# Performance work log

Measured on AMD Instinct MI355X. Metric: run time of the kernel, lower is better.

The kernel has to match this reference:

```python
import jax, jax.numpy as jnp
import numpy as np

B, N, IN_F, OUT_F = 32, 1024, 256, 256
ALPHA = 0.2  # LeakyReLU negative slope
NEG_INF = -9e15  # matches torch's -9000000000000000.0 masking constant


def setup_inputs() -> dict:
    key = jax.random.key(0)
    k1, k2, k3, k4 = jax.random.split(key, 4)
    h = jax.random.normal(k1, (B, N, IN_F), dtype=jnp.float32)
    adj = jax.random.randint(k2, (B, N, N), 0, 2, dtype=jnp.int32)
    W = jax.random.normal(k3, (OUT_F, IN_F), dtype=jnp.float32) * 0.05
    a = jax.random.normal(k4, (1, 2 * OUT_F), dtype=jnp.float32) * 0.05
    return {"h": h, "adj": adj, "W": W, "a": a}


def reference(h, adj, W, a):
    # Wh: (B, N, out)
    Wh = jnp.einsum("bni,oi->bno", h, W)
    # Decompose a([Wh_i || Wh_j]) = Wh_i . a1 + Wh_j . a2 (identical math,
    # avoids the O(B*N^2*2*out) concat intermediate of the torch code).
    a1 = a[0, :OUT_F]   # (out,)
    a2 = a[0, OUT_F:]   # (out,)
    si = Wh @ a1        # (B, N) score contribution of source node i
    sj = Wh @ a2        # (B, N) score contribution of neighbor node j
    e = jax.nn.leaky_relu(si[:, :, None] + sj[:, None, :], negative_slope=ALPHA)
    attention = jnp.where(adj > 0, e, NEG_INF)
    attention = jax.nn.softmax(attention, axis=-1)
    # dropout omitted (eval mode)
    h_prime = jnp.einsum("bij,bjo->bio", attention, Wh)
    return jax.nn.elu(h_prime)
```

## Files before the change

kernel.cpp:

```cpp
#include <hip/hip_runtime.h>
#include <hip/hip_bf16.h>


#define ALPHA 0.2f

typedef __bf16 bf16x8 __attribute__((ext_vector_type(8)));
typedef __bf16 bf16x4 __attribute__((ext_vector_type(4)));
typedef float  f32x4  __attribute__((ext_vector_type(4)));
typedef unsigned long long u64;

__global__ __launch_bounds__(256) void k0_mask(const int* __restrict__ adj,
                                               u64* __restrict__ mask) {
    const int wid = (blockIdx.x * 256 + threadIdx.x) >> 6;
    const int l   = threadIdx.x & 63;
    const size_t base = (size_t)wid * 64;
    #pragma unroll 4
    for (int it = 0; it < 64; ++it) {
        const size_t word = base + it;
        const int v = adj[word * 64 + l];
        const u64 m = __ballot(v > 0);
        if (l == 0) mask[word] = m;
    }
}

__global__ __launch_bounds__(256) void k1_gemm1(const float* __restrict__ h,
                                                const float* __restrict__ W,
                                                const float* __restrict__ a_g,
                                                __bf16* __restrict__ whT,
                                                float* __restrict__ si,
                                                float* __restrict__ sj) {
    __shared__ __bf16 hA[64 * 72];
    __shared__ __bf16 hB[256 * 72];
    __shared__ float  red[512];
    const int t    = threadIdx.x;
    const int r0   = blockIdx.x * 64;
    const int b    = r0 >> 10;
    const int n0   = r0 & 1023;
    const int w    = t >> 6;
    const int l    = t & 63;
    const int ln   = l & 15;
    const int quad = l >> 4;

    f32x4 acc[4][4] = {};
    float4 ha_r[4], wb_r[16];

    #pragma unroll
    for (int it = 0; it < 4; ++it)
        ha_r[it] = *(const float4*)&h[(size_t)(r0 + it * 16 + (t >> 4)) * 256 + (t & 15) * 4];
    #pragma unroll
    for (int it = 0; it < 16; ++it)
        wb_r[it] = *(const float4*)&W[(size_t)(it * 16 + (t >> 4)) * 256 + (t & 15) * 4];

    for (int kc = 0; kc < 4; ++kc) {
        #pragma unroll
        for (int it = 0; it < 4; ++it) {
            const float4 v = ha_r[it];
            bf16x4 pv = {(__bf16)v.x, (__bf16)v.y, (__bf16)v.z, (__bf16)v.w};
            *(bf16x4*)&hA[(it * 16 + (t >> 4)) * 72 + (t & 15) * 4] = pv;
        }
        #pragma unroll
        for (int it = 0; it < 16; ++it) {
            const float4 v = wb_r[it];
            bf16x4 pv = {(__bf16)v.x, (__bf16)v.y, (__bf16)v.z, (__bf16)v.w};
            *(bf16x4*)&hB[(it * 16 + (t >> 4)) * 72 + (t & 15) * 4] = pv;
        }
        __syncthreads();
        if (kc < 3) {
            const int k0 = (kc + 1) * 64;
            #pragma unroll
            for (int it = 0; it < 4; ++it)
                ha_r[it] = *(const float4*)&h[(size_t)(r0 + it * 16 + (t >> 4)) * 256 + k0 + (t & 15) * 4];
            #pragma unroll
            for (int it = 0; it < 16; ++it)
                wb_r[it] = *(const float4*)&W[(size_t)(it * 16 + (t >> 4)) * 256 + k0 + (t & 15) * 4];
        }
        #pragma unroll
        for (int kk = 0; kk < 2; ++kk) {
            bf16x8 af[4], bfr[4];
            #pragma unroll
            for (int ri = 0; ri < 4; ++ri)
                af[ri] = *(const bf16x8*)&hA[(ri * 16 + ln) * 72 + kk * 32 + quad * 8];
            #pragma unroll
            for (int oi = 0; oi < 4; ++oi)
                bfr[oi] = *(const bf16x8*)&hB[(w * 64 + oi * 16 + ln) * 72 + kk * 32 + quad * 8];
            #pragma unroll
            for (int ri = 0; ri < 4; ++ri)
                #pragma unroll
                for (int oi = 0; oi < 4; ++oi)
                    acc[ri][oi] = __builtin_amdgcn_mfma_f32_16x16x32_bf16(
                        af[ri], bfr[oi], acc[ri][oi], 0, 0, 0);
        }
        __syncthreads();
    }

    #pragma unroll
    for (int ri = 0; ri < 4; ++ri) {
        const int n = ri * 16 + quad * 4;
        #pragma unroll
        for (int oi = 0; oi < 4; ++oi) {
            const int o = w * 64 + oi * 16 + ln;
            bf16x4 pv = {(__bf16)acc[ri][oi][0], (__bf16)acc[ri][oi][1],
                         (__bf16)acc[ri][oi][2], (__bf16)acc[ri][oi][3]};
            *(bf16x4*)&hB[o * 72 + n] = pv;
        }
    }
    __syncthreads();

    #pragma unroll
    for (int it = 0; it < 8; ++it) {
        const int o   = w * 64 + it * 8 + (l >> 3);
        const int seg = l & 7;
        const bf16x8 v = *(const bf16x8*)&hB[o * 72 + seg * 8];
        *(bf16x8*)&whT[((size_t)b * 256 + o) * 1024 + n0 + seg * 8] = v;
    }

    {
        float s1 = 0.f, s2 = 0.f;
        #pragma unroll 8
        for (int oi = 0; oi < 64; ++oi) {
            const int o = w * 64 + oi;
            const float v = (float)hB[o * 72 + l];
            s1 += v * a_g[o];
            s2 += v * a_g[256 + o];
        }
        red[w * 64 + l]       = s1;
        red[256 + w * 64 + l] = s2;
    }
    __syncthreads();
    if (t < 64) {
        si[b * 1024 + n0 + t] = red[t] + red[64 + t] + red[128 + t] + red[192 + t];
    } else if (t < 128) {
        const int n = t - 64;
        sj[b * 1024 + n0 + n] = red[256 + n] + red[320 + n] + red[384 + n] + red[448 + n];
    }
}

__global__ __launch_bounds__(256) void k3_attn(const u64* __restrict__ mask,
                                               const __bf16* __restrict__ whT,
                                               const float* __restrict__ si_g,
                                               const float* __restrict__ sj_g,
                                               float* __restrict__ out) {
    __shared__ __bf16 lds_w[256 * 72];
    __shared__ __bf16 lds_s[64 * 72];
    __shared__ float  lds_denom[64];
    const int t    = threadIdx.x;
    const int b    = blockIdx.y;
    const int i0   = blockIdx.x * 64;
    const int w    = t >> 6;
    const int l    = t & 63;
    const int ln   = l & 15;
    const int quad = l >> 4;
    const int g    = t >> 4;
    const int j4   = t & 15;

    float si_r[4];
    #pragma unroll
    for (int m = 0; m < 4; ++m) si_r[m] = si_g[b * 1024 + i0 + m * 16 + g];

    float dsum[4] = {0.f, 0.f, 0.f, 0.f};
    f32x4 acc[4][4] = {};
    const __bf16* whTb  = whT + (size_t)b * 256 * 1024;
    const u64*    maskb = mask + ((size_t)b * 1024) * 16;

    bf16x8 vreg[8];
    u64    msk[4];
    float4 sjv;

    #pragma unroll
    for (int it = 0; it < 8; ++it)
        vreg[it] = *(const bf16x8*)&whTb[(size_t)(it * 32 + (t >> 3)) * 1024 + (t & 7) * 8];
    #pragma unroll
    for (int m = 0; m < 4; ++m) msk[m] = maskb[(size_t)(i0 + m * 16 + g) * 16];
    sjv = *(const float4*)&sj_g[b * 1024 + j4 * 4];

    for (int jc = 0; jc < 16; ++jc) {
        const int j0 = jc * 64;
        #pragma unroll
        for (int it = 0; it < 8; ++it)
            *(bf16x8*)&lds_w[(it * 32 + (t >> 3)) * 72 + (t & 7) * 8] = vreg[it];
        #pragma unroll
        for (int m = 0; m < 4; ++m) {
            const int il   = m * 16 + g;
            const unsigned bits = (unsigned)(msk[m] >> (4 * j4)) & 0xFu;
            float e0 = si_r[m] + sjv.x; e0 = e0 > 0.f ? e0 : ALPHA * e0;
            float e1 = si_r[m] + sjv.y; e1 = e1 > 0.f ? e1 : ALPHA * e1;
            float e2 = si_r[m] + sjv.z; e2 = e2 > 0.f ? e2 : ALPHA * e2;
            float e3 = si_r[m] + sjv.w; e3 = e3 > 0.f ? e3 : ALPHA * e3;
            const float w0 = (bits & 1u) ? __expf(e0) : 0.f;
            const float w1 = (bits & 2u) ? __expf(e1) : 0.f;
            const float w2 = (bits & 4u) ? __expf(e2) : 0.f;
            const float w3 = (bits & 8u) ? __expf(e3) : 0.f;
            bf16x4 pv = {(__bf16)w0, (__bf16)w1, (__bf16)w2, (__bf16)w3};
            dsum[m] += (float)pv[0] + (float)pv[1] + (float)pv[2] + (float)pv[3];
            *(bf16x4*)&lds_s[il * 72 + j4 * 4] = pv;
        }
        __syncthreads();
        if (jc < 15) {
            const int j1 = j0 + 64;
            #pragma unroll
            for (int it = 0; it < 8; ++it)
                vreg[it] = *(const bf16x8*)&whTb[(size_t)(it * 32 + (t >> 3)) * 1024 + j1 + (t & 7) * 8];
            #pragma unroll
            for (int m = 0; m < 4; ++m)
                msk[m] = maskb[(size_t)(i0 + m * 16 + g) * 16 + jc + 1];
            sjv = *(const float4*)&sj_g[b * 1024 + j1 + j4 * 4];
        }
        #pragma unroll
        for (int kk = 0; kk < 2; ++kk) {
            bf16x8 af[4], bfr[4];
            #pragma unroll
            for (int ri = 0; ri < 4; ++ri)
                af[ri] = *(const bf16x8*)&lds_s[(ri * 16 + ln) * 72 + kk * 32 + quad * 8];
            #pragma unroll
            for (int oi = 0; oi < 4; ++oi)
                bfr[oi] = *(const bf16x8*)&lds_w[(w * 64 + oi * 16 + ln) * 72 + kk * 32 + quad * 8];
            #pragma unroll
            for (int ri = 0; ri < 4; ++ri)
                #pragma unroll
                for (int oi = 0; oi < 4; ++oi)
                    acc[ri][oi] = __builtin_amdgcn_mfma_f32_16x16x32_bf16(
                        af[ri], bfr[oi], acc[ri][oi], 0, 0, 0);
        }
        __syncthreads();
    }

    #pragma unroll
    for (int m = 0; m < 4; ++m) {
        float v = dsum[m];
        v += __shfl_xor(v, 1);
        v += __shfl_xor(v, 2);
        v += __shfl_xor(v, 4);
        v += __shfl_xor(v, 8);
        if (j4 == 0) lds_denom[m * 16 + g] = v;
    }
    __syncthreads();
    #pragma unroll
    for (int ri = 0; ri < 4; ++ri) {
        #pragma unroll
        for (int q = 0; q < 4; ++q) {
            const int il = ri * 16 + quad * 4 + q;
            const float dinv = 1.0f / fmaxf(lds_denom[il], 1e-30f);
            #pragma unroll
            for (int oi = 0; oi < 4; ++oi) {
                const int o = w * 64 + oi * 16 + ln;
                const float v = acc[ri][oi][q] * dinv;
                const float r = v > 0.f ? v : __expf(v) - 1.f;
                out[((size_t)(b * 1024 + i0 + il)) * 256 + o] = r;
            }
        }
    }
}

extern "C" void kernel_launch(void* const* d_in, const int* in_sizes, int n_in,
                              void* d_out, int out_size, void* d_ws, size_t ws_size,
                              hipStream_t stream) {
    const float* h   = (const float*)d_in[0];
    const int*   adj = (const int*)d_in[1];
    const float* W   = (const float*)d_in[2];
    const float* a   = (const float*)d_in[3];
    float* out = (float*)d_out;

    __bf16* whT  = (__bf16*)d_ws;
    float*  si   = (float*)((char*)d_ws + (size_t)16777216);
    float*  sj   = (float*)((char*)d_ws + (size_t)16777216 + 131072);
    u64*    mask = (u64*)((char*)d_ws + (size_t)16777216 + 262144);

    k0_mask<<<2048, 256, 0, stream>>>(adj, mask);
    k1_gemm1<<<512, 256, 0, stream>>>(h, W, a, whT, si, sj);
    k3_attn<<<dim3(16, 32), 256, 0, stream>>>(mask, whT, si, sj, out);
}
```

Baseline: 285.4 us.

## Fuse adjacency mask into attention kernel and read Wh fragments directly from global

Drops the separate bitmask-packing kernel and has the attention kernel read int32 adjacency directly with int4 loads, prefetched one chunk ahead. Wh B-fragments are now loaded straight from global into registers instead of being staged through LDS. The score LDS buffer is double-buffered so one barrier per iteration suffices. Scores are pre-scaled by log2(e) so exp2f can be used, and blocks are remapped so neighbouring workgroups spread across batches. The cost is that each attention block rereads its 256KB adjacency tile at full int32 width, and Wh global reads are no longer shared through LDS.

```diff
diff --git a/kernel.cpp b/kernel.cpp
--- a/kernel.cpp
+++ b/kernel.cpp
@@ -3,25 +3,12 @@
 
 
 #define ALPHA 0.2f
+#define LOG2E 1.44269504f
 
 typedef __bf16 bf16x8 __attribute__((ext_vector_type(8)));
 typedef __bf16 bf16x4 __attribute__((ext_vector_type(4)));
 typedef float  f32x4  __attribute__((ext_vector_type(4)));
 typedef unsigned long long u64;
-
-__global__ __launch_bounds__(256) void k0_mask(const int* __restrict__ adj,
-                                               u64* __restrict__ mask) {
-    const int wid = (blockIdx.x * 256 + threadIdx.x) >> 6;
-    const int l   = threadIdx.x & 63;
-    const size_t base = (size_t)wid * 64;
-    #pragma unroll 4
-    for (int it = 0; it < 64; ++it) {
-        const size_t word = base + it;
-        const int v = adj[word * 64 + l];
-        const u64 m = __ballot(v > 0);
-        if (l == 0) mask[word] = m;
-    }
-}
 
 __global__ __launch_bounds__(256) void k1_gemm1(const float* __restrict__ h,
                                                 const float* __restrict__ W,
@@ -128,24 +115,27 @@
     }
     __syncthreads();
     if (t < 64) {
-        si[b * 1024 + n0 + t] = red[t] + red[64 + t] + red[128 + t] + red[192 + t];
+        si[b * 1024 + n0 + t] =
+            (red[t] + red[64 + t] + red[128 + t] + red[192 + t]) * LOG2E;
     } else if (t < 128) {
         const int n = t - 64;
-        sj[b * 1024 + n0 + n] = red[256 + n] + red[320 + n] + red[384 + n] + red[448 + n];
+        sj[b * 1024 + n0 + n] =
+            (red[256 + n] + red[320 + n] + red[384 + n] + red[448 + n]) * LOG2E;
     }
 }
 
-__global__ __launch_bounds__(256) void k3_attn(const u64* __restrict__ mask,
+__global__ __launch_bounds__(256) void k3_attn(const int* __restrict__ adj,
                                                const __bf16* __restrict__ whT,
                                                const float* __restrict__ si_g,
                                                const float* __restrict__ sj_g,
                                                float* __restrict__ out) {
-    __shared__ __bf16 lds_w[256 * 72];
-    __shared__ __bf16 lds_s[64 * 72];
+    __shared__ __bf16 lds_s[2][64 * 72];
     __shared__ float  lds_denom[64];
-    const int t    = threadIdx.x;
-    const int b    = blockIdx.y;
-    const int i0   = blockIdx.x * 64;
+    const int t = threadIdx.x;
+    const int orig = blockIdx.x;
+    const int wgid = (orig & 7) * 64 + (orig >> 3);
+    const int b    = wgid >> 4;
+    const int i0   = (wgid & 15) << 6;
     const int w    = t >> 6;
     const int l    = t & 63;
     const int ln   = l & 15;
@@ -159,69 +149,66 @@
 
     float dsum[4] = {0.f, 0.f, 0.f, 0.f};
     f32x4 acc[4][4] = {};
-    const __bf16* whTb  = whT + (size_t)b * 256 * 1024;
-    const u64*    maskb = mask + ((size_t)b * 1024) * 16;
-
-    bf16x8 vreg[8];
-    u64    msk[4];
+    const __bf16* whTb = whT + (size_t)b * 256 * 1024;
+    const int*    adjb = adj + ((size_t)(b * 1024 + i0)) * 1024;
+
+    int4   amsk[4];
     float4 sjv;
-
-    #pragma unroll
-    for (int it = 0; it < 8; ++it)
-        vreg[it] = *(const bf16x8*)&whTb[(size_t)(it * 32 + (t >> 3)) * 1024 + (t & 7) * 8];
-    #pragma unroll
-    for (int m = 0; m < 4; ++m) msk[m] = maskb[(size_t)(i0 + m * 16 + g) * 16];
+    #pragma unroll
+    for (int m = 0; m < 4; ++m)
+        amsk[m] = *(const int4*)&adjb[(size_t)(m * 16 + g) * 1024 + j4 * 4];
     sjv = *(const float4*)&sj_g[b * 1024 + j4 * 4];
 
+    #pragma unroll 2
     for (int jc = 0; jc < 16; ++jc) {
         const int j0 = jc * 64;
-        #pragma unroll
-        for (int it = 0; it < 8; ++it)
-            *(bf16x8*)&lds_w[(it * 32 + (t >> 3)) * 72 + (t & 7) * 8] = vreg[it];
+        __bf16* s_buf = (__bf16*)lds_s[jc & 1];
+
+        bf16x8 bfr[2][4];
+        #pragma unroll
+        for (int kk = 0; kk < 2; ++kk)
+            #pragma unroll
+            for (int oi = 0; oi < 4; ++oi)
+                bfr[kk][oi] = *(const bf16x8*)&whTb[
+                    (size_t)(w * 64 + oi * 16 + ln) * 1024 + j0 + kk * 32 + quad * 8];
+
         #pragma unroll
         for (int m = 0; m < 4; ++m) {
-            const int il   = m * 16 + g;
-            const unsigned bits = (unsigned)(msk[m] >> (4 * j4)) & 0xFu;
+            const int il = m * 16 + g;
             float e0 = si_r[m] + sjv.x; e0 = e0 > 0.f ? e0 : ALPHA * e0;
             float e1 = si_r[m] + sjv.y; e1 = e1 > 0.f ? e1 : ALPHA * e1;
             float e2 = si_r[m] + sjv.z; e2 = e2 > 0.f ? e2 : ALPHA * e2;
             float e3 = si_r[m] + sjv.w; e3 = e3 > 0.f ? e3 : ALPHA * e3;
-            const float w0 = (bits & 1u) ? __expf(e0) : 0.f;
-            const float w1 = (bits & 2u) ? __expf(e1) : 0.f;
-            const float w2 = (bits & 4u) ? __expf(e2) : 0.f;
-            const float w3 = (bits & 8u) ? __expf(e3) : 0.f;
+            const float w0 = amsk[m].x > 0 ? exp2f(e0) : 0.f;
+            const float w1 = amsk[m].y > 0 ? exp2f(e1) : 0.f;
+            const float w2 = amsk[m].z > 0 ? exp2f(e2) : 0.f;
+            const float w3 = amsk[m].w > 0 ? exp2f(e3) : 0.f;
             bf16x4 pv = {(__bf16)w0, (__bf16)w1, (__bf16)w2, (__bf16)w3};
             dsum[m] += (float)pv[0] + (float)pv[1] + (float)pv[2] + (float)pv[3];
-            *(bf16x4*)&lds_s[il * 72 + j4 * 4] = pv;
+            *(bf16x4*)&s_buf[il * 72 + j4 * 4] = pv;
+        }
+
+        if (jc < 15) {
+            #pragma unroll
+            for (int m = 0; m < 4; ++m)
+                amsk[m] = *(const int4*)&adjb[(size_t)(m * 16 + g) * 1024 + j0 + 64 + j4 * 4];
+            sjv = *(const float4*)&sj_g[b * 1024 + j0 + 64 + j4 * 4];
         }
         __syncthreads();
-        if (jc < 15) {
-            const int j1 = j0 + 64;
-            #pragma unroll
-            for (int it = 0; it < 8; ++it)
-                vreg[it] = *(const bf16x8*)&whTb[(size_t)(it * 32 + (t >> 3)) * 1024 + j1 + (t & 7) * 8];
-            #pragma unroll
-            for (int m = 0; m < 4; ++m)
-                msk[m] = maskb[(size_t)(i0 + m * 16 + g) * 16 + jc + 1];
-            sjv = *(const float4*)&sj_g[b * 1024 + j1 + j4 * 4];
-        }
+
         #pragma unroll
         for (int kk = 0; kk < 2; ++kk) {
-            bf16x8 af[4], bfr[4];
-            #pragma unroll
-            for (int ri = 0; ri < 4; ++ri)
-                af[ri] = *(const bf16x8*)&lds_s[(ri * 16 + ln) * 72 + kk * 32 + quad * 8];
-            #pragma unroll
-            for (int oi = 0; oi < 4; ++oi)
-                bfr[oi] = *(const bf16x8*)&lds_w[(w * 64 + oi * 16 + ln) * 72 + kk * 32 + quad * 8];
+            bf16x8 af[4];
+            #pragma unroll
+            for (int ri = 0; ri < 4; ++ri)
+                af[ri] = *(const bf16x8*)&s_buf[(ri * 16 + ln) * 72 + kk * 32 + quad * 8];
             #pragma unroll
             for (int ri = 0; ri < 4; ++ri)
                 #pragma unroll
                 for (int oi = 0; oi < 4; ++oi)
                     acc[ri][oi] = __builtin_amdgcn_mfma_f32_16x16x32_bf16(
-                        af[ri], bfr[oi], acc[ri][oi], 0, 0, 0);
-        }
-        __syncthreads();
+                        af[ri], bfr[kk][oi], acc[ri][oi], 0, 0, 0);
+        }
     }
 
     #pragma unroll
@@ -260,12 +247,10 @@
     const float* a   = (const float*)d_in[3];
     float* out = (float*)d_out;
 
-    __bf16* whT  = (__bf16*)d_ws;
-    float*  si   = (float*)((char*)d_ws + (size_t)16777216);
-    float*  sj   = (float*)((char*)d_ws + (size_t)16777216 + 131072);
-    u64*    mask = (u64*)((char*)d_ws + (size_t)16777216 + 262144);
-
-    k0_mask<<<2048, 256, 0, stream>>>(adj, mask);
+    __bf16* whT = (__bf16*)d_ws;
+    float*  si  = (float*)((char*)d_ws + (size_t)16777216);
+    float*  sj  = (float*)((char*)d_ws + (size_t)16777216 + 131072);
+
     k1_gemm1<<<512, 256, 0, stream>>>(h, W, a, whT, si, sj);
-    k3_attn<<<dim3(16, 32), 256, 0, stream>>>(mask, whT, si, sj, out);
+    k3_attn<<<512, 256, 0, stream>>>(adj, whT, si, sj, out);
 }
```

Result: faster. 257.4 us (-9.8%).
